# Performance work log

Hardware: AMD Instinct MI355X
Metric: run time of the kernel (lower is better)

## Reference

```python
import jax, jax.numpy as jnp
import numpy as np

THRESHOLD = 0.01
TOPK_RATIO = 0.7

def setup_inputs() -> dict:
    key = jax.random.key(0)
    k1, k2, k3, k4, k5 = jax.random.split(key, 5)
    B, N, F, K = 8, 2048, 512, 256
    x = jax.random.normal(k1, (B, N, F), dtype=jnp.float32)
    adj = jax.random.uniform(k2, (B, N, N), dtype=jnp.float32)
    mask = jnp.ones((B, N), dtype=jnp.float32)
    # assign_main = Linear(F->K), ReLU, Linear(K->K)
    W1 = jax.random.normal(k3, (F, K), dtype=jnp.float32) / np.sqrt(F)
    b1 = jnp.zeros((K,), dtype=jnp.float32)
    W2 = jax.random.normal(k4, (K, K), dtype=jnp.float32) / np.sqrt(K)
    b2 = jnp.zeros((K,), dtype=jnp.float32)
    return {"x": x, "adj": adj, "mask": mask, "W1": W1, "b1": b1, "W2": W2, "b2": b2}

def reference(x, adj, mask, W1, b1, W2, b2):
    B, N, Fdim = x.shape
    K = W2.shape[1]
    # soft assignment logits with masked softmax over clusters
    h = jax.nn.relu(jnp.einsum('bnf,fk->bnk', x, W1) + b1)
    logits = jnp.einsum('bnk,kl->bnl', h, W2) + b2            # [B,N,K]
    logits = logits + (-1e9) * (1.0 - mask[..., None])
    S = jax.nn.softmax(logits, axis=-1)                       # [B,N,K]
    # pooled features and pooled adjacency
    pfeat = jnp.einsum('bnk,bnf->bkf', S, x)                  # S^T x -> [B,K,F]
    mid = jnp.einsum('bnm,bmk->bnk', adj, S)                  # adj @ S
    pooled = jnp.einsum('bnk,bnl->bkl', S, mid)               # S^T adj S -> [B,K,K]
    # threshold + top-k sparsify with straight-through estimator
    topk = min(K, int(np.ceil(TOPK_RATIO * K)))
    thr_mask = (pooled >= THRESHOLD).astype(pooled.dtype)
    a_thr = pooled * thr_mask
    _, idx = jax.lax.top_k(a_thr, topk)                       # [B,K,topk]
    bi = jnp.arange(B)[:, None, None]
    ri = jnp.arange(K)[None, :, None]
    fmask = jnp.zeros_like(pooled).at[bi, ri, idx].set(1.0)
    a_sp = pooled * fmask
    a_ste = a_sp + jax.lax.stop_gradient(pooled - a_sp)       # forward == pooled
    # symmetric degree renormalization
    row_sum = a_ste.sum(axis=-1)
    d_inv_sqrt = 1.0 / jnp.sqrt(row_sum + 1e-9)
    pooled_adj = a_ste * d_inv_sqrt[:, :, None] * d_inv_sqrt[:, None, :]
    pmask = jnp.ones((B, K), dtype=x.dtype)
    return pfeat, pooled_adj, pmask
```

## Files before the change

### kernel.cpp

```cpp
#include <hip/hip_runtime.h>
#include <hip/hip_bf16.h>


typedef float f32x4 __attribute__((ext_vector_type(4)));
typedef __bf16 bf16x8 __attribute__((ext_vector_type(8)));

#define VMCNT(n) asm volatile("s_waitcnt vmcnt(" #n ")" ::: "memory")
#define LGKM0    asm volatile("s_waitcnt lgkmcnt(0)" ::: "memory")
#define SCHEDB   __builtin_amdgcn_sched_barrier(0)
#define BARRIER                                        \
  do {                                                 \
    LGKM0;                                             \
    __builtin_amdgcn_s_barrier();                      \
    asm volatile("" ::: "memory");                     \
    SCHEDB;                                            \
  } while (0)

__device__ __forceinline__ void async_load16(const void* g, void* l) {
  __builtin_amdgcn_global_load_lds((const __attribute__((address_space(1))) void*)g,
                                   (__attribute__((address_space(3))) void*)l, 16, 0, 0);
}
__device__ __forceinline__ unsigned short f2bf(float f) {
  return __builtin_bit_cast(unsigned short, (__bf16)f);
}
__device__ __forceinline__ ushort4 f4_to_bf4(float4 v) {
  ushort4 u; u.x = f2bf(v.x); u.y = f2bf(v.y); u.z = f2bf(v.z); u.w = f2bf(v.w); return u;
}

template <int ROWS, int BK, int NT>
__device__ __forceinline__ void stage_bf16(const __bf16* __restrict__ src, long long ld,
                                           __bf16* lds, int t) {
  constexpr int GR = BK / 8;
  constexpr int N = ROWS * GR / NT;
  static_assert(N >= 1, "stage too small");
#pragma unroll
  for (int c = 0; c < N; ++c) {
    const int idx = c * NT + t;
    const int row = idx / GR;
    const int g = idx % GR;
    const int gs = g ^ (row & (GR - 1) & 7);
    async_load16(src + (long long)row * ld + gs * 8, lds + idx * 8);
  }
}
template <int BK>
__device__ __forceinline__ bf16x8 frag(const __bf16* lds, int row, int kq) {
  constexpr int GR = BK / 8;
  const int g = kq ^ (row & (GR - 1) & 7);
  return *(const bf16x8*)(lds + row * BK + g * 8);
}

__global__ __launch_bounds__(256) void prep_k(const float* __restrict__ x,
                                              const float* __restrict__ W1,
                                              const float* __restrict__ W2,
                                              __bf16* __restrict__ xbT,
                                              __bf16* __restrict__ W1T,
                                              __bf16* __restrict__ W2T) {
  __shared__ float tile[64][65];
  const int tr = threadIdx.x >> 6, tc = threadIdx.x & 63;
  const int bid = blockIdx.x;
  const float* in; __bf16* out; int r0, c0, C, R;
  if (bid < 2048) {
    const int fb = bid >> 8, rest = bid & 255;
    const int nb = rest >> 3, b = rest & 7;
    in = x + (long long)b * 1048576; out = xbT + (long long)b * 1048576;
    r0 = nb * 64; c0 = fb * 64; R = 2048; C = 512;
  } else if (bid < 2080) {
    const int w = bid - 2048;
    in = W1; out = W1T; r0 = (w >> 2) * 64; c0 = (w & 3) * 64; R = 512; C = 256;
  } else {
    const int w = bid - 2080;
    in = W2; out = W2T; r0 = (w >> 2) * 64; c0 = (w & 3) * 64; R = 256; C = 256;
  }
#pragma unroll
  for (int i = 0; i < 16; ++i)
    tile[tr + i * 4][tc] = in[(long long)(r0 + tr + i * 4) * C + c0 + tc];
  __syncthreads();
#pragma unroll
  for (int i = 0; i < 16; ++i)
    out[(long long)(c0 + tr + i * 4) * R + r0 + tc] = (__bf16)tile[tc][tr + i * 4];
}

__device__ __forceinline__ void asg_compute(const __bf16* __restrict__ Abuf,
                                            const __bf16* __restrict__ Bbuf,
                                            f32x4 (&acc)[2][4], int wn, int l15, int l4) {
  bf16x8 af[2], bf[4];
#pragma unroll
  for (int i = 0; i < 2; ++i) af[i] = frag<32>(Abuf, i * 16 + l15, l4);
#pragma unroll
  for (int j = 0; j < 4; ++j) bf[j] = frag<32>(Bbuf, wn + j * 16 + l15, l4);
  __builtin_amdgcn_s_setprio(1);
#pragma unroll
  for (int i = 0; i < 2; ++i)
#pragma unroll
    for (int j = 0; j < 4; ++j)
      acc[i][j] = __builtin_amdgcn_mfma_f32_16x16x32_bf16(af[i], bf[j], acc[i][j], 0, 0, 0);
  __builtin_amdgcn_s_setprio(0);
}

__global__ __launch_bounds__(256) void assign_fused_k(
    const float* __restrict__ x, const __bf16* __restrict__ W1T,
    const __bf16* __restrict__ W2T, const float* __restrict__ b1,
    const float* __restrict__ b2, const float* __restrict__ mask,
    __bf16* __restrict__ ST) {
  __shared__ alignas(16) __bf16 Ax[2][32 * 32];
  __shared__ alignas(16) __bf16 Bw[2][256 * 32];
  __shared__ alignas(16) __bf16 hl[32 * 264];
  __shared__ float red[2][4][32];

  const int t = threadIdx.x;
  const int lane = t & 63, wave = t >> 6;
  const int l15 = lane & 15, l4 = lane >> 4;
  const int wn = wave * 64;
  const long long row0 = (long long)blockIdx.x * 32;
  const float* Xb = x + row0 * 512;

  const int arow = t >> 3, afq = t & 7;
  const int ag = afq >> 1;
  const int aoff = arow * 32 + ((ag ^ (arow & 3)) * 8) + (afq & 1) * 4;

  auto ldx = [&](int tile) -> float4 {
    return *(const float4*)(Xb + (long long)arow * 512 + tile * 32 + afq * 4);
  };
  auto sta = [&](__bf16* dst, float4 v) { *(ushort4*)&dst[aoff] = f4_to_bf4(v); };

  f32x4 acc[2][4] = {};

  float4 xA = ldx(0);
  SCHEDB;
  stage_bf16<256, 32, 256>(W1T, 512, Bw[0], t);
  SCHEDB;
  VMCNT(4); SCHEDB;
  sta(Ax[0], xA);
  float4 xB = ldx(1);
  SCHEDB;
  VMCNT(1); SCHEDB;
  BARRIER;

#pragma unroll 1
  for (int tt = 0; tt < 14; tt += 2) {
    stage_bf16<256, 32, 256>(W1T + (tt + 1) * 32, 512, Bw[1], t);
    SCHEDB;
    xA = ldx(tt + 2);
    SCHEDB;
    asg_compute(Ax[0], Bw[0], acc, wn, l15, l4);
    VMCNT(5); SCHEDB;
    sta(Ax[1], xB);
    VMCNT(1); SCHEDB;
    BARRIER;
    stage_bf16<256, 32, 256>(W1T + (tt + 2) * 32, 512, Bw[0], t);
    SCHEDB;
    xB = ldx(tt + 3);
    SCHEDB;
    asg_compute(Ax[1], Bw[1], acc, wn, l15, l4);
    VMCNT(5); SCHEDB;
    sta(Ax[0], xA);
    VMCNT(1); SCHEDB;
    BARRIER;
  }
  stage_bf16<256, 32, 256>(W1T + 15 * 32, 512, Bw[1], t);
  SCHEDB;
  asg_compute(Ax[0], Bw[0], acc, wn, l15, l4);
  VMCNT(4); SCHEDB;
  sta(Ax[1], xB);
  VMCNT(0); SCHEDB;
  BARRIER;
  asg_compute(Ax[1], Bw[1], acc, wn, l15, l4);

  stage_bf16<256, 32, 256>(W2T, 256, Bw[0], t);
  SCHEDB;
#pragma unroll
  for (int j = 0; j < 4; ++j) {
    const int col = wn + j * 16 + l15;
    const float bv = b1[col];
#pragma unroll
    for (int i = 0; i < 2; ++i)
#pragma unroll
      for (int r = 0; r < 4; ++r)
        hl[(i * 16 + l4 * 4 + r) * 264 + col] = (__bf16)fmaxf(acc[i][j][r] + bv, 0.f);
  }
  VMCNT(0); SCHEDB;
  BARRIER;

  f32x4 acc2[2][4] = {};
#pragma unroll 1
  for (int tt = 0; tt < 8; ++tt) {
    if (tt < 7) stage_bf16<256, 32, 256>(W2T + (tt + 1) * 32, 256, Bw[(tt & 1) ^ 1], t);
    SCHEDB;
    const __bf16* Bc = Bw[tt & 1];
    bf16x8 af[2], bf[4];
#pragma unroll
    for (int i = 0; i < 2; ++i)
      af[i] = *(const bf16x8*)(&hl[(i * 16 + l15) * 264 + tt * 32 + l4 * 8]);
#pragma unroll
    for (int j = 0; j < 4; ++j) bf[j] = frag<32>(Bc, wn + j * 16 + l15, l4);
#pragma unroll
    for (int i = 0; i < 2; ++i)
#pragma unroll
      for (int j = 0; j < 4; ++j)
        acc2[i][j] = __builtin_amdgcn_mfma_f32_16x16x32_bf16(af[i], bf[j], acc2[i][j], 0, 0, 0);
    VMCNT(0); SCHEDB;
    BARRIER;
  }

  float mb[2][4], mx[2][4], sm[2][4];
#pragma unroll
  for (int i = 0; i < 2; ++i)
#pragma unroll
    for (int r = 0; r < 4; ++r) {
      mb[i][r] = -1e9f * (1.0f - mask[row0 + i * 16 + l4 * 4 + r]);
      mx[i][r] = -3.4e38f;
      sm[i][r] = 0.f;
    }
#pragma unroll
  for (int j = 0; j < 4; ++j) {
    const float bv = b2[wn + j * 16 + l15];
#pragma unroll
    for (int i = 0; i < 2; ++i)
#pragma unroll
      for (int r = 0; r < 4; ++r) {
        const float v = acc2[i][j][r] + bv + mb[i][r];
        acc2[i][j][r] = v;
        mx[i][r] = fmaxf(mx[i][r], v);
      }
  }
#pragma unroll
  for (int i = 0; i < 2; ++i)
#pragma unroll
    for (int r = 0; r < 4; ++r) {
      float m = mx[i][r];
      m = fmaxf(m, __shfl_xor(m, 1, 64)); m = fmaxf(m, __shfl_xor(m, 2, 64));
      m = fmaxf(m, __shfl_xor(m, 4, 64)); m = fmaxf(m, __shfl_xor(m, 8, 64));
      mx[i][r] = m;
    }
  if (l15 == 0)
#pragma unroll
    for (int i = 0; i < 2; ++i)
#pragma unroll
      for (int r = 0; r < 4; ++r) red[0][wave][i * 16 + l4 * 4 + r] = mx[i][r];
  __syncthreads();
#pragma unroll
  for (int i = 0; i < 2; ++i)
#pragma unroll
    for (int r = 0; r < 4; ++r) {
      const int rl = i * 16 + l4 * 4 + r;
      mx[i][r] = fmaxf(fmaxf(red[0][0][rl], red[0][1][rl]),
                       fmaxf(red[0][2][rl], red[0][3][rl]));
    }
#pragma unroll
  for (int j = 0; j < 4; ++j)
#pragma unroll
    for (int i = 0; i < 2; ++i)
#pragma unroll
      for (int r = 0; r < 4; ++r) {
        const float e = __expf(acc2[i][j][r] - mx[i][r]);
        acc2[i][j][r] = e;
        sm[i][r] += e;
      }
#pragma unroll
  for (int i = 0; i < 2; ++i)
#pragma unroll
    for (int r = 0; r < 4; ++r) {
      float s = sm[i][r];
      s += __shfl_xor(s, 1, 64); s += __shfl_xor(s, 2, 64);
      s += __shfl_xor(s, 4, 64); s += __shfl_xor(s, 8, 64);
      sm[i][r] = s;
    }
  if (l15 == 0)
#pragma unroll
    for (int i = 0; i < 2; ++i)
#pragma unroll
      for (int r = 0; r < 4; ++r) red[1][wave][i * 16 + l4 * 4 + r] = sm[i][r];
  __syncthreads();
  float inv[2][4];
#pragma unroll
  for (int i = 0; i < 2; ++i)
#pragma unroll
    for (int r = 0; r < 4; ++r) {
      const int rl = i * 16 + l4 * 4 + r;
      inv[i][r] = 1.0f / (red[1][0][rl] + red[1][1][rl] + red[1][2][rl] + red[1][3][rl]);
    }
  const long long bb = row0 >> 11;
  const long long n0 = row0 & 2047;
  __bf16* Sb = ST + bb * 524288;
#pragma unroll
  for (int j = 0; j < 4; ++j) {
    const int col = wn + j * 16 + l15;
#pragma unroll
    for (int i = 0; i < 2; ++i) {
      ushort4 u;
      u.x = f2bf(acc2[i][j][0] * inv[i][0]);
      u.y = f2bf(acc2[i][j][1] * inv[i][1]);
      u.z = f2bf(acc2[i][j][2] * inv[i][2]);
      u.w = f2bf(acc2[i][j][3] * inv[i][3]);
      *(ushort4*)(Sb + (long long)col * 2048 + n0 + i * 16 + l4 * 4) = u;
    }
  }
}

__global__ __launch_bounds__(512) void gemm_adj_k(const float* __restrict__ adj,
                                                  const __bf16* __restrict__ ST,
                                                  __bf16* __restrict__ midT) {
  __shared__ alignas(16) __bf16 Aa[2][64 * 64];
  __shared__ alignas(16) __bf16 Bs[3][256 * 64];
  const int t = threadIdx.x;
  const int lane = t & 63, wave = t >> 6;
  const int l15 = lane & 15, l4 = lane >> 4;
  const int wr = (wave >> 2) * 32;
  const int wc = (wave & 3) * 64;
  const int id = blockIdx.x;
  const int bz = id & 7;
  const long long r0 = (long long)(id >> 3) * 64;
  const float* Ab = adj + (long long)bz * 4194304 + r0 * 2048;
  const __bf16* Bb = ST + (long long)bz * 524288;

  const int arow = t >> 4, afq = t & 15;
  auto ldA = [&](int tile, float4 (&r)[2]) {
#pragma unroll
    for (int c = 0; c < 2; ++c)
      r[c] = *(const float4*)(Ab + (long long)(arow + c * 32) * 2048 + tile * 64 + afq * 4);
  };
  auto stA = [&](__bf16* dst, const float4 (&r)[2]) {
#pragma unroll
    for (int c = 0; c < 2; ++c) {
      const int row = arow + c * 32;
      const int off = row * 64 + (((afq >> 1) ^ (row & 7)) * 8) + (afq & 1) * 4;
      *(ushort4*)&dst[off] = f4_to_bf4(r[c]);
    }
  };

  f32x4 acc[2][4] = {};
  float4 rA[2], rB[2];

  auto cmp = [&](const __bf16* Ac, const __bf16* Bc) {
#pragma unroll
    for (int ks = 0; ks < 2; ++ks) {
      bf16x8 af[2], bf[4];
#pragma unroll
      for (int i = 0; i < 2; ++i) af[i] = frag<64>(Ac, wr + i * 16 + l15, ks * 4 + l4);
#pragma unroll
      for (int j = 0; j < 4; ++j) bf[j] = frag<64>(Bc, wc + j * 16 + l15, ks * 4 + l4);
      __builtin_amdgcn_s_setprio(1);
#pragma unroll
      for (int i = 0; i < 2; ++i)
#pragma unroll
        for (int j = 0; j < 4; ++j)
          acc[i][j] = __builtin_amdgcn_mfma_f32_16x16x32_bf16(af[i], bf[j], acc[i][j], 0, 0, 0);
      __builtin_amdgcn_s_setprio(0);
    }
  };

  stage_bf16<256, 64, 512>(Bb, 2048, Bs[0], t);
  SCHEDB;
  ldA(0, rA);
  SCHEDB;
  stage_bf16<256, 64, 512>(Bb + 64, 2048, Bs[1], t);
  SCHEDB;
  ldA(1, rB);
  SCHEDB;
  VMCNT(6); SCHEDB;
  stA(Aa[0], rA);
  BARRIER;

  int curB = 0, stgB = 2;
#pragma unroll 1
  for (int tt = 0; tt < 30; tt += 2) {
    stage_bf16<256, 64, 512>(Bb + (tt + 2) * 64, 2048, Bs[stgB], t);
    SCHEDB;
    ldA(tt + 2, rA);
    SCHEDB;
    cmp(Aa[0], Bs[curB]);
    VMCNT(6); SCHEDB;
    stA(Aa[1], rB);
    BARRIER;
    curB = (curB == 2) ? 0 : curB + 1;
    stgB = (stgB == 2) ? 0 : stgB + 1;
    stage_bf16<256, 64, 512>(Bb + (tt + 3) * 64, 2048, Bs[stgB], t);
    SCHEDB;
    ldA(tt + 3, rB);
    SCHEDB;
    cmp(Aa[1], Bs[curB]);
    VMCNT(6); SCHEDB;
    stA(Aa[0], rA);
    BARRIER;
    curB = (curB == 2) ? 0 : curB + 1;
    stgB = (stgB == 2) ? 0 : stgB + 1;
  }
  cmp(Aa[0], Bs[curB]);
  VMCNT(0); SCHEDB;
  stA(Aa[1], rB);
  BARRIER;
  curB = (curB == 2) ? 0 : curB + 1;
  cmp(Aa[1], Bs[curB]);

  __bf16* Cb = midT + (long long)bz * 524288;
#pragma unroll
  for (int j = 0; j < 4; ++j) {
    const int l = wc + j * 16 + l15;
#pragma unroll
    for (int i = 0; i < 2; ++i) {
      ushort4 u;
      u.x = f2bf(acc[i][j][0]); u.y = f2bf(acc[i][j][1]);
      u.z = f2bf(acc[i][j][2]); u.w = f2bf(acc[i][j][3]);
      *(ushort4*)(Cb + (long long)l * 2048 + r0 + wr + i * 16 + l4 * 4) = u;
    }
  }
}

__global__ __launch_bounds__(256) void gemm_feat_k(const __bf16* __restrict__ ST,
                                                   const __bf16* __restrict__ xbT,
                                                   float* __restrict__ pfeat) {
  __shared__ alignas(16) __bf16 As[3][32 * 64];
  __shared__ alignas(16) __bf16 Bs[3][64 * 64];
  const int t = threadIdx.x;
  const int lane = t & 63, wave = t >> 6;
  const int l15 = lane & 15, l4 = lane >> 4;
  const int wn = wave * 16;
  const int id = blockIdx.x;
  const int b = id & 7, j7 = id >> 3;
  const int kblk = j7 & 7, fblk = j7 >> 3;
  const __bf16* Ab = ST + (long long)b * 524288 + (long long)kblk * 32 * 2048;
  const __bf16* Bb = xbT + (long long)b * 1048576 + (long long)fblk * 64 * 2048;

  auto stage = [&](int s, int buf) {
    stage_bf16<32, 64, 256>(Ab + s * 64, 2048, (__bf16*)As + buf * 2048, t);
    stage_bf16<64, 64, 256>(Bb + s * 64, 2048, (__bf16*)Bs + buf * 4096, t);
  };
  auto cmp = [&](int buf, f32x4 (&acc)[2]) {
    const __bf16* Ac = (const __bf16*)As + buf * 2048;
    const __bf16* Bc = (const __bf16*)Bs + buf * 4096;
#pragma unroll
    for (int ks = 0; ks < 2; ++ks) {
      bf16x8 af[2], bf;
#pragma unroll
      for (int i = 0; i < 2; ++i) af[i] = frag<64>(Ac, i * 16 + l15, ks * 4 + l4);
      bf = frag<64>(Bc, wn + l15, ks * 4 + l4);
#pragma unroll
      for (int i = 0; i < 2; ++i)
        acc[i] = __builtin_amdgcn_mfma_f32_16x16x32_bf16(af[i], bf, acc[i], 0, 0, 0);
    }
  };

  f32x4 acc[2] = {};
  stage(0, 0);
  SCHEDB;
  stage(1, 1);
  SCHEDB;
  VMCNT(3); SCHEDB;
  BARRIER;

  int cur = 0, stg = 2;
#pragma unroll 1
  for (int tt = 0; tt < 30; ++tt) {
    stage(tt + 2, stg);
    SCHEDB;
    cmp(cur, acc);
    VMCNT(3); SCHEDB;
    BARRIER;
    cur = (cur == 2) ? 0 : cur + 1;
    stg = (stg == 2) ? 0 : stg + 1;
  }
  cmp(cur, acc);
  VMCNT(0); SCHEDB;
  BARRIER;
  cur = (cur == 2) ? 0 : cur + 1;
  cmp(cur, acc);

  float* out = pfeat + (long long)b * 131072;
#pragma unroll
  for (int i = 0; i < 2; ++i)
#pragma unroll
    for (int r = 0; r < 4; ++r)
      out[(long long)(kblk * 32 + i * 16 + l4 * 4 + r) * 512 + fblk * 64 + wn + l15] =
          acc[i][r];
}

__global__ __launch_bounds__(256) void gemm_pool_k(const __bf16* __restrict__ ST,
                                                   const __bf16* __restrict__ midT,
                                                   float* __restrict__ pooled) {
  __shared__ alignas(16) __bf16 As[3][32 * 64];
  __shared__ alignas(16) __bf16 Bs[3][32 * 64];
  const int t = threadIdx.x;
  const int lane = t & 63, wave = t >> 6;
  const int l15 = lane & 15, l4 = lane >> 4;
  const int wm = (wave >> 1) * 16, wn = (wave & 1) * 16;
  const int id = blockIdx.x;
  const int b = id & 7, j7 = id >> 3;
  const int kblk = j7 & 7, lblk = j7 >> 3;
  const __bf16* Ab = ST + (long long)b * 524288 + (long long)kblk * 32 * 2048;
  const __bf16* Bb = midT + (long long)b * 524288 + (long long)lblk * 32 * 2048;

  auto stage = [&](int s, int buf) {
    stage_bf16<32, 64, 256>(Ab + s * 64, 2048, (__bf16*)As + buf * 2048, t);
    stage_bf16<32, 64, 256>(Bb + s * 64, 2048, (__bf16*)Bs + buf * 2048, t);
  };
  auto cmp = [&](int buf, f32x4& acc) {
    const __bf16* Ac = (const __bf16*)As + buf * 2048;
    const __bf16* Bc = (const __bf16*)Bs + buf * 2048;
#pragma unroll
    for (int ks = 0; ks < 2; ++ks) {
      bf16x8 af = frag<64>(Ac, wm + l15, ks * 4 + l4);
      bf16x8 bf = frag<64>(Bc, wn + l15, ks * 4 + l4);
      acc = __builtin_amdgcn_mfma_f32_16x16x32_bf16(af, bf, acc, 0, 0, 0);
    }
  };

  f32x4 acc = {};
  stage(0, 0);
  SCHEDB;
  stage(1, 1);
  SCHEDB;
  VMCNT(2); SCHEDB;
  BARRIER;

  int cur = 0, stg = 2;
#pragma unroll 1
  for (int tt = 0; tt < 30; ++tt) {
    stage(tt + 2, stg);
    SCHEDB;
    cmp(cur, acc);
    VMCNT(2); SCHEDB;
    BARRIER;
    cur = (cur == 2) ? 0 : cur + 1;
    stg = (stg == 2) ? 0 : stg + 1;
  }
  cmp(cur, acc);
  VMCNT(0); SCHEDB;
  BARRIER;
  cur = (cur == 2) ? 0 : cur + 1;
  cmp(cur, acc);

  float* out = pooled + (long long)b * 65536;
#pragma unroll
  for (int r = 0; r < 4; ++r)
    out[(long long)(kblk * 32 + wm + l4 * 4 + r) * 256 + lblk * 32 + wn + l15] = acc[r];
}

__global__ __launch_bounds__(256) void rowsum_k(const float* __restrict__ pooled,
                                                float* __restrict__ dinv) {
  const int gr = blockIdx.x * 4 + (threadIdx.x >> 6);
  const int lane = threadIdx.x & 63;
  const float* p = pooled + (long long)gr * 256;
  float s = p[lane] + p[lane + 64] + p[lane + 128] + p[lane + 192];
#pragma unroll
  for (int o = 32; o > 0; o >>= 1) s += __shfl_xor(s, o, 64);
  if (lane == 0) dinv[gr] = rsqrtf(s + 1e-9f);
}

__global__ __launch_bounds__(256) void finalize_k(const float* __restrict__ pooled,
                                                  const float* __restrict__ dinv,
                                                  float* __restrict__ outAdj,
                                                  float* __restrict__ pmask) {
  const long long i = blockIdx.x * 256LL + threadIdx.x;
  const int c = (int)(i & 255);
  const int r = (int)((i >> 8) & 255);
  const int b = (int)(i >> 16);
  outAdj[i] = pooled[i] * dinv[b * 256 + r] * dinv[b * 256 + c];
  if (i < 2048) pmask[i] = 1.0f;
}

extern "C" void kernel_launch(void* const* d_in, const int* in_sizes, int n_in,
                              void* d_out, int out_size, void* d_ws, size_t ws_size,
                              hipStream_t stream) {
  (void)in_sizes; (void)n_in; (void)out_size; (void)ws_size;
  const float* x    = (const float*)d_in[0];
  const float* adj  = (const float*)d_in[1];
  const float* mask = (const float*)d_in[2];
  const float* W1   = (const float*)d_in[3];
  const float* b1   = (const float*)d_in[4];
  const float* W2   = (const float*)d_in[5];
  const float* b2   = (const float*)d_in[6];

  char* ws = (char*)d_ws;
  __bf16* ST     = (__bf16*)(ws + 0);
  __bf16* midT   = (__bf16*)(ws + 8388608);
  __bf16* xbT    = (__bf16*)(ws + 16777216);
  float*  pooled = (float*)(ws + 33554432);
  float*  dinv   = (float*)(ws + 35651584);
  __bf16* W1T    = (__bf16*)(ws + 35659776);
  __bf16* W2T    = (__bf16*)(ws + 35921920);

  float* pfeat  = (float*)d_out;
  float* outAdj = (float*)d_out + 1048576;
  float* pmask  = (float*)d_out + 1572864;

  prep_k<<<2096, 256, 0, stream>>>(x, W1, W2, xbT, W1T, W2T);
  assign_fused_k<<<512, 256, 0, stream>>>(x, W1T, W2T, b1, b2, mask, ST);
  gemm_feat_k<<<512, 256, 0, stream>>>(ST, xbT, pfeat);
  gemm_adj_k<<<256, 512, 0, stream>>>(adj, ST, midT);
  gemm_pool_k<<<512, 256, 0, stream>>>(ST, midT, pooled);
  rowsum_k<<<512, 256, 0, stream>>>(pooled, dinv);
  finalize_k<<<2048, 256, 0, stream>>>(pooled, dinv, outAdj, pmask);
}
```

Baseline: 118.5 us.

## Run adj@S GEMM in FP8 with scaled S copy

The assignment kernel now also writes an FP8 copy of S, scaled by 64, and the adjacency GEMM converts adj tiles to FP8 and uses FP8 MFMA instructions instead of BF16, rescaling the result at the end. This halves LDS and global traffic for the S operand and the LDS footprint for both operands. The adj read from global memory stays FP32, so the dominant bandwidth cost is unchanged. It adds an extra FP8 write in the assignment kernel and reduces precision of the pooled adjacency, which could affect top-k and threshold decisions.

```diff
diff --git a/kernel.cpp b/kernel.cpp
--- a/kernel.cpp
+++ b/kernel.cpp
@@ -26,6 +26,11 @@
 __device__ __forceinline__ ushort4 f4_to_bf4(float4 v) {
   ushort4 u; u.x = f2bf(v.x); u.y = f2bf(v.y); u.z = f2bf(v.z); u.w = f2bf(v.w); return u;
 }
+__device__ __forceinline__ int f4_to_fp8x4(float a, float b, float c, float d) {
+  int w = __builtin_amdgcn_cvt_pk_fp8_f32(a, b, 0, false);
+  w = __builtin_amdgcn_cvt_pk_fp8_f32(c, d, w, true);
+  return w;
+}
 
 template <int ROWS, int BK, int NT>
 __device__ __forceinline__ void stage_bf16(const __bf16* __restrict__ src, long long ld,
@@ -47,6 +52,26 @@
   constexpr int GR = BK / 8;
   const int g = kq ^ (row & (GR - 1) & 7);
   return *(const bf16x8*)(lds + row * BK + g * 8);
+}
+
+template <int ROWS, int NT>
+__device__ __forceinline__ void stage_fp8(const unsigned char* __restrict__ src,
+                                          long long ld, unsigned char* lds, int t) {
+  constexpr int GR = 4;
+  constexpr int N = ROWS * GR / NT;
+  static_assert(N >= 1, "stage too small");
+#pragma unroll
+  for (int c = 0; c < N; ++c) {
+    const int idx = c * NT + t;
+    const int row = idx / GR;
+    const int g = idx % GR;
+    const int gs = g ^ ((row >> 1) & 3);
+    async_load16(src + (long long)row * ld + gs * 16, lds + idx * 16);
+  }
+}
+__device__ __forceinline__ long frag8(const unsigned char* lds, int row, int kq) {
+  const int slot = (kq >> 1) ^ ((row >> 1) & 3);
+  return *(const long*)(lds + row * 64 + slot * 16 + (kq & 1) * 8);
 }
 
 __global__ __launch_bounds__(256) void prep_k(const float* __restrict__ x,
@@ -101,7 +126,7 @@
     const float* __restrict__ x, const __bf16* __restrict__ W1T,
     const __bf16* __restrict__ W2T, const float* __restrict__ b1,
     const float* __restrict__ b2, const float* __restrict__ mask,
-    __bf16* __restrict__ ST) {
+    __bf16* __restrict__ ST, unsigned char* __restrict__ ST8) {
   __shared__ alignas(16) __bf16 Ax[2][32 * 32];
   __shared__ alignas(16) __bf16 Bw[2][256 * 32];
   __shared__ alignas(16) __bf16 hl[32 * 264];
@@ -282,26 +307,30 @@
   const long long bb = row0 >> 11;
   const long long n0 = row0 & 2047;
   __bf16* Sb = ST + bb * 524288;
+  unsigned char* S8 = ST8 + bb * 524288;
 #pragma unroll
   for (int j = 0; j < 4; ++j) {
     const int col = wn + j * 16 + l15;
 #pragma unroll
     for (int i = 0; i < 2; ++i) {
+      const float v0 = acc2[i][j][0] * inv[i][0];
+      const float v1 = acc2[i][j][1] * inv[i][1];
+      const float v2 = acc2[i][j][2] * inv[i][2];
+      const float v3 = acc2[i][j][3] * inv[i][3];
       ushort4 u;
-      u.x = f2bf(acc2[i][j][0] * inv[i][0]);
-      u.y = f2bf(acc2[i][j][1] * inv[i][1]);
-      u.z = f2bf(acc2[i][j][2] * inv[i][2]);
-      u.w = f2bf(acc2[i][j][3] * inv[i][3]);
+      u.x = f2bf(v0); u.y = f2bf(v1); u.z = f2bf(v2); u.w = f2bf(v3);
       *(ushort4*)(Sb + (long long)col * 2048 + n0 + i * 16 + l4 * 4) = u;
+      *(int*)(S8 + (long long)col * 2048 + n0 + i * 16 + l4 * 4) =
+          f4_to_fp8x4(v0 * 64.f, v1 * 64.f, v2 * 64.f, v3 * 64.f);
     }
   }
 }
 
 __global__ __launch_bounds__(512) void gemm_adj_k(const float* __restrict__ adj,
-                                                  const __bf16* __restrict__ ST,
+                                                  const unsigned char* __restrict__ ST8,
                                                   __bf16* __restrict__ midT) {
-  __shared__ alignas(16) __bf16 Aa[2][64 * 64];
-  __shared__ alignas(16) __bf16 Bs[3][256 * 64];
+  __shared__ alignas(16) unsigned char Aa[2][64 * 64];
+  __shared__ alignas(16) unsigned char Bs[3][256 * 64];
   const int t = threadIdx.x;
   const int lane = t & 63, wave = t >> 6;
   const int l15 = lane & 15, l4 = lane >> 4;
@@ -311,75 +340,76 @@
   const int bz = id & 7;
   const long long r0 = (long long)(id >> 3) * 64;
   const float* Ab = adj + (long long)bz * 4194304 + r0 * 2048;
-  const __bf16* Bb = ST + (long long)bz * 524288;
-
-  const int arow = t >> 4, afq = t & 15;
+  const unsigned char* Bb = ST8 + (long long)bz * 524288;
+
+  const int arow = t >> 3, ak = t & 7;
+  const int aoff = arow * 64 + ((((ak >> 1) ^ ((arow >> 1) & 3))) << 4) + (ak & 1) * 8;
   auto ldA = [&](int tile, float4 (&r)[2]) {
-#pragma unroll
-    for (int c = 0; c < 2; ++c)
-      r[c] = *(const float4*)(Ab + (long long)(arow + c * 32) * 2048 + tile * 64 + afq * 4);
-  };
-  auto stA = [&](__bf16* dst, const float4 (&r)[2]) {
-#pragma unroll
-    for (int c = 0; c < 2; ++c) {
-      const int row = arow + c * 32;
-      const int off = row * 64 + (((afq >> 1) ^ (row & 7)) * 8) + (afq & 1) * 4;
-      *(ushort4*)&dst[off] = f4_to_bf4(r[c]);
-    }
+    const float* p = Ab + (long long)arow * 2048 + tile * 64 + ak * 8;
+    r[0] = *(const float4*)p;
+    r[1] = *(const float4*)(p + 4);
+  };
+  auto stA = [&](unsigned char* dst, const float4 (&r)[2]) {
+    int2 w;
+    w.x = f4_to_fp8x4(r[0].x, r[0].y, r[0].z, r[0].w);
+    w.y = f4_to_fp8x4(r[1].x, r[1].y, r[1].z, r[1].w);
+    *(long*)(dst + aoff) = __builtin_bit_cast(long, w);
   };
 
   f32x4 acc[2][4] = {};
   float4 rA[2], rB[2];
 
-  auto cmp = [&](const __bf16* Ac, const __bf16* Bc) {
-#pragma unroll
-    for (int ks = 0; ks < 2; ++ks) {
-      bf16x8 af[2], bf[4];
-#pragma unroll
-      for (int i = 0; i < 2; ++i) af[i] = frag<64>(Ac, wr + i * 16 + l15, ks * 4 + l4);
-#pragma unroll
-      for (int j = 0; j < 4; ++j) bf[j] = frag<64>(Bc, wc + j * 16 + l15, ks * 4 + l4);
+  auto cmp = [&](const unsigned char* Ac, const unsigned char* Bc) {
+#pragma unroll
+    for (int m = 0; m < 2; ++m) {
+      const int kq = m * 4 + l4;
+      long af[2], bf[4];
+#pragma unroll
+      for (int i = 0; i < 2; ++i) af[i] = frag8(Ac, wr + i * 16 + l15, kq);
+#pragma unroll
+      for (int j = 0; j < 4; ++j) bf[j] = frag8(Bc, wc + j * 16 + l15, kq);
       __builtin_amdgcn_s_setprio(1);
 #pragma unroll
       for (int i = 0; i < 2; ++i)
 #pragma unroll
         for (int j = 0; j < 4; ++j)
-          acc[i][j] = __builtin_amdgcn_mfma_f32_16x16x32_bf16(af[i], bf[j], acc[i][j], 0, 0, 0);
+          acc[i][j] =
+              __builtin_amdgcn_mfma_f32_16x16x32_fp8_fp8(af[i], bf[j], acc[i][j], 0, 0, 0);
       __builtin_amdgcn_s_setprio(0);
     }
   };
 
-  stage_bf16<256, 64, 512>(Bb, 2048, Bs[0], t);
+  stage_fp8<256, 512>(Bb, 2048, Bs[0], t);
   SCHEDB;
   ldA(0, rA);
   SCHEDB;
-  stage_bf16<256, 64, 512>(Bb + 64, 2048, Bs[1], t);
+  stage_fp8<256, 512>(Bb + 64, 2048, Bs[1], t);
   SCHEDB;
   ldA(1, rB);
   SCHEDB;
-  VMCNT(6); SCHEDB;
+  VMCNT(4); SCHEDB;
   stA(Aa[0], rA);
   BARRIER;
 
   int curB = 0, stgB = 2;
 #pragma unroll 1
   for (int tt = 0; tt < 30; tt += 2) {
-    stage_bf16<256, 64, 512>(Bb + (tt + 2) * 64, 2048, Bs[stgB], t);
+    stage_fp8<256, 512>(Bb + (tt + 2) * 64, 2048, Bs[stgB], t);
     SCHEDB;
     ldA(tt + 2, rA);
     SCHEDB;
     cmp(Aa[0], Bs[curB]);
-    VMCNT(6); SCHEDB;
+    VMCNT(4); SCHEDB;
     stA(Aa[1], rB);
     BARRIER;
     curB = (curB == 2) ? 0 : curB + 1;
     stgB = (stgB == 2) ? 0 : stgB + 1;
-    stage_bf16<256, 64, 512>(Bb + (tt + 3) * 64, 2048, Bs[stgB], t);
+    stage_fp8<256, 512>(Bb + (tt + 3) * 64, 2048, Bs[stgB], t);
     SCHEDB;
     ldA(tt + 3, rB);
     SCHEDB;
     cmp(Aa[1], Bs[curB]);
-    VMCNT(6); SCHEDB;
+    VMCNT(4); SCHEDB;
     stA(Aa[0], rA);
     BARRIER;
     curB = (curB == 2) ? 0 : curB + 1;
@@ -393,14 +423,15 @@
   cmp(Aa[1], Bs[curB]);
 
   __bf16* Cb = midT + (long long)bz * 524288;
+  const float sc = 1.0f / 64.0f;
 #pragma unroll
   for (int j = 0; j < 4; ++j) {
     const int l = wc + j * 16 + l15;
 #pragma unroll
     for (int i = 0; i < 2; ++i) {
       ushort4 u;
-      u.x = f2bf(acc[i][j][0]); u.y = f2bf(acc[i][j][1]);
-      u.z = f2bf(acc[i][j][2]); u.w = f2bf(acc[i][j][3]);
+      u.x = f2bf(acc[i][j][0] * sc); u.y = f2bf(acc[i][j][1] * sc);
+      u.z = f2bf(acc[i][j][2] * sc); u.w = f2bf(acc[i][j][3] * sc);
       *(ushort4*)(Cb + (long long)l * 2048 + r0 + wr + i * 16 + l4 * 4) = u;
     }
   }
@@ -578,15 +609,16 @@
   float*  dinv   = (float*)(ws + 35651584);
   __bf16* W1T    = (__bf16*)(ws + 35659776);
   __bf16* W2T    = (__bf16*)(ws + 35921920);
+  unsigned char* ST8 = (unsigned char*)(ws + 36052992);
 
   float* pfeat  = (float*)d_out;
   float* outAdj = (float*)d_out + 1048576;
   float* pmask  = (float*)d_out + 1572864;
 
   prep_k<<<2096, 256, 0, stream>>>(x, W1, W2, xbT, W1T, W2T);
-  assign_fused_k<<<512, 256, 0, stream>>>(x, W1T, W2T, b1, b2, mask, ST);
+  assign_fused_k<<<512, 256, 0, stream>>>(x, W1T, W2T, b1, b2, mask, ST, ST8);
   gemm_feat_k<<<512, 256, 0, stream>>>(ST, xbT, pfeat);
-  gemm_adj_k<<<256, 512, 0, stream>>>(adj, ST, midT);
+  gemm_adj_k<<<256, 512, 0, stream>>>(adj, ST8, midT);
   gemm_pool_k<<<512, 256, 0, stream>>>(ST, midT, pooled);
   rowsum_k<<<512, 256, 0, stream>>>(pooled, dinv);
   finalize_k<<<2048, 256, 0, stream>>>(pooled, dinv, outAdj, pmask);
```

Result: no change. 116.3 us (-1.8%).
